# Kernel tuning notes

Measured on AMD Instinct MI355X. Metric: run time of the kernel, lower is better.

Reference implementation:

```python
import jax, jax.numpy as jnp
import numpy as np

def setup_inputs() -> dict:
    key = jax.random.key(0)
    k1, k2, k3 = jax.random.split(key, 3)
    B, L, H, E = 2, 2048, 16, 64
    queries = jax.random.normal(k1, (B, L, H, E), dtype=jnp.float32)
    keys = jax.random.normal(k2, (B, L, H, E), dtype=jnp.float32)
    values = jax.random.normal(k3, (B, L, H, E), dtype=jnp.float32)
    return {"queries": queries, "keys": keys, "values": values}

def reference(queries, keys, values):
    B, L, H, E = queries.shape
    S = keys.shape[1]
    scale = 1.0 / jnp.sqrt(jnp.asarray(E, dtype=queries.dtype))
    # scores: [B, H, L, S]
    scores = jnp.einsum('blhe,bshe->bhls', queries, keys)
    # causal mask: position l attends to s <= l (TriangularCausalMask triu diag=1 is masked)
    causal = jnp.tril(jnp.ones((L, S), dtype=bool))  # True = keep
    scores = jnp.where(causal[None, None, :, :], scores, -jnp.inf)
    A = jax.nn.softmax(scale * scores, axis=-1)
    # dropout is identity in eval / p=0
    V = jnp.einsum('bhls,bshd->blhd', A, values)
    return V
```

## Files before the change

kernel.cpp:

```cpp
#include <hip/hip_runtime.h>
#include <hip/hip_bf16.h>

typedef __attribute__((ext_vector_type(8))) short short8;
typedef __attribute__((ext_vector_type(4))) float f32x4;
typedef __attribute__((ext_vector_type(2))) unsigned uint2v;

#define MFMA16(a, b, c) __builtin_amdgcn_mfma_f32_16x16x32_bf16((a), (b), (c), 0, 0, 0)

constexpr int Bc = 2, Lc = 2048, Hc = 16, Ec = 64;
constexpr float LOG2E = 1.4426950408889634f;
constexpr float SCALE2 = 0.125f * LOG2E;
constexpr float NEGBIG = -3.0e38f;

union SW { short8 s8; unsigned u[4]; float4 f4; };

__device__ __forceinline__ unsigned cvtpk(float lo, float hi) {
  unsigned r;
  asm("v_cvt_pk_bf16_f32 %0, %1, %2" : "=v"(r) : "v"(lo), "v"(hi));
  return r;
}
__device__ __forceinline__ float exp2v(float x) {
  float r;
  asm("v_exp_f32 %0, %1" : "=v"(r) : "v"(x));
  return r;
}
__device__ __forceinline__ void plswap32(unsigned& a, unsigned& b) {
  uint2v r = __builtin_amdgcn_permlane32_swap(a, b, false, false);
  a = r[0]; b = r[1];
}
__device__ __forceinline__ void plswap16(unsigned& a, unsigned& b) {
  uint2v r = __builtin_amdgcn_permlane16_swap(a, b, false, false);
  a = r[0]; b = r[1];
}
__device__ __forceinline__ float bflymax(float x) {
  unsigned a = __builtin_bit_cast(unsigned, x), b = a;
  plswap16(a, b);
  float y = fmaxf(__builtin_bit_cast(float, a), __builtin_bit_cast(float, b));
  a = __builtin_bit_cast(unsigned, y); b = a;
  plswap32(a, b);
  return fmaxf(__builtin_bit_cast(float, a), __builtin_bit_cast(float, b));
}

__global__ __launch_bounds__(256)
void prep(const float* __restrict__ K, const float* __restrict__ V,
          uint4* __restrict__ Kb, unsigned short* __restrict__ Vt) {
  const int bid = blockIdx.x;
  const int t = threadIdx.x;
  if (bid < 2048) {
    const int i = bid * 256 + t;
    const float4* s = reinterpret_cast<const float4*>(K) + (size_t)i * 2;
    float4 a = s[0], b = s[1];
    uint4 o;
    o.x = cvtpk(a.x, a.y); o.y = cvtpk(a.z, a.w);
    o.z = cvtpk(b.x, b.y); o.w = cvtpk(b.z, b.w);
    Kb[i] = o;
  } else {
    const int vw = (bid - 2048) * 4 + (t >> 6);
    const int l = t & 63;
    const int bh = vw >> 7;
    const int s0 = (vw & 127) * 16;
    const float* vp = V + ((size_t)(bh >> 4) * Lc + s0) * (Hc * Ec) +
                      (bh & 15) * Ec + l;
    float va[16];
    #pragma unroll
    for (int j = 0; j < 16; ++j) va[j] = vp[j * (Hc * Ec)];
    uint4 o0, o1;
    o0.x = cvtpk(va[0], va[1]);   o0.y = cvtpk(va[2], va[3]);
    o0.z = cvtpk(va[4], va[5]);   o0.w = cvtpk(va[6], va[7]);
    o1.x = cvtpk(va[8], va[9]);   o1.y = cvtpk(va[10], va[11]);
    o1.z = cvtpk(va[12], va[13]); o1.w = cvtpk(va[14], va[15]);
    uint4* dst = reinterpret_cast<uint4*>(Vt + ((size_t)vw * 64 + l) * 16);
    dst[0] = o0;
    dst[1] = o1;
  }
}

__global__ __launch_bounds__(512, 2)
void attn_fwd(const float* __restrict__ Qg, const unsigned short* __restrict__ Kb,
              const unsigned short* __restrict__ Vt, float* __restrict__ Og) {
  __shared__ __align__(16) short kt2[2][8192];
  __shared__ __align__(16) float mscr[64 * 68 + 128];

  const int bid = blockIdx.x;
  const int pair = bid >> 5;
  const int bh = bid & 31;
  const int h = bh & (Hc - 1);
  const int b = bh >> 4;
  const int iLo = pair;
  const int QbL = iLo * 64;
  const int QbH = (31 - pair) * 64;
  const int RL = (iLo + 2) >> 1;

  const int t = threadIdx.x;
  const int w = t >> 6;
  const int qsub = w & 3;
  const int par = w >> 2;
  const int l = t & 63;
  const int n = l & 15;
  const int g = l >> 4;
  const int sp4 = ((g & 1) << 3) | ((g >> 1) << 2);

  const f32x4 zero4 = {0.f, 0.f, 0.f, 0.f};
  short8 onesv;
  #pragma unroll
  for (int j = 0; j < 8; ++j) onesv[j] = (short)0x3F80;

  short8 qf[2];
  auto loadq = [&](int Qb) {
    const int q = Qb + qsub * 16 + n;
    const float* qp = Qg + ((size_t)(b * Lc + q) * Hc + h) * Ec + g * 8;
    SW a0, a1, b0, b1, r0, r1;
    a0.f4 = reinterpret_cast<const float4*>(qp)[0];
    a1.f4 = reinterpret_cast<const float4*>(qp)[1];
    b0.f4 = reinterpret_cast<const float4*>(qp + 32)[0];
    b1.f4 = reinterpret_cast<const float4*>(qp + 32)[1];
    r0.u[0] = cvtpk(a0.f4.x * SCALE2, a0.f4.y * SCALE2);
    r0.u[1] = cvtpk(a0.f4.z * SCALE2, a0.f4.w * SCALE2);
    r0.u[2] = cvtpk(a1.f4.x * SCALE2, a1.f4.y * SCALE2);
    r0.u[3] = cvtpk(a1.f4.z * SCALE2, a1.f4.w * SCALE2);
    r1.u[0] = cvtpk(b0.f4.x * SCALE2, b0.f4.y * SCALE2);
    r1.u[1] = cvtpk(b0.f4.z * SCALE2, b0.f4.w * SCALE2);
    r1.u[2] = cvtpk(b1.f4.x * SCALE2, b1.f4.y * SCALE2);
    r1.u[3] = cvtpk(b1.f4.z * SCALE2, b1.f4.w * SCALE2);
    qf[0] = r0.s8;
    qf[1] = r1.s8;
  };

  f32x4 acc[4] = {zero4, zero4, zero4, zero4};
  float mrun = NEGBIG, lrun = 0.f;

  const int srow = t >> 2;
  const int prow = (srow & ~12) | ((srow & 4) << 1) | ((srow & 8) >> 1);
  const int kc0 = (t & 3) * 16;

  float4 kA, kB;

  auto issueK = [&](int r0) {
    unsigned koff = (unsigned)((((b * Lc + r0 + srow) * Hc + h) * Ec + kc0) * 2);
    asm volatile(
      "global_load_dwordx4 %[k0], %[ko], %[kb]\n\t"
      "global_load_dwordx4 %[k1], %[ko], %[kb] offset:16"
      : [k0]"=v"(kA), [k1]"=v"(kB)
      : [ko]"v"(koff), [kb]"s"(Kb)
      : "memory");
  };
  auto commit = [&](int buf) {
    asm volatile("s_waitcnt vmcnt(0)" ::: "memory");
    __builtin_amdgcn_sched_barrier(0);
    short* kt = kt2[buf];
    *reinterpret_cast<short8*>(&kt[(prow * 64 + kc0) ^ ((prow & 7) << 3)]) =
        *reinterpret_cast<short8*>(&kA);
    *reinterpret_cast<short8*>(&kt[(prow * 64 + kc0 + 8) ^ ((prow & 7) << 3)]) =
        *reinterpret_cast<short8*>(&kB);
  };

  auto round = [&](int Qb, int str, int curb, bool pre, int nstrK) {
    const int sb = str * 128 + par * 64;
    const int qtop = Qb + qsub * 16;
    if (sb > qtop + 15) {
      if (pre) issueK(nstrK * 128);
      return;
    }
    const short* ktb = kt2[curb];

    f32x4 sc[4] = {zero4, zero4, zero4, zero4};
    __builtin_amdgcn_s_setprio(1);
    #pragma unroll
    for (int kc = 0; kc < 2; ++kc) {
      #pragma unroll
      for (int cb = 0; cb < 4; ++cb) {
        const int row = par * 64 + cb * 16 + n;
        const int idx = (row * 64 + kc * 32 + g * 8) ^ ((n & 7) << 3);
        short8 kf = *reinterpret_cast<const short8*>(&ktb[idx]);
        sc[cb] = MFMA16(kf, qf[kc], sc[cb]);
      }
    }
    __builtin_amdgcn_s_setprio(0);

    SW vr0[4], vr1[4];
    {
      unsigned a0 = (unsigned)((((bh * 128 + str * 8 + par * 4 + (g >> 1)) * 64 + n) * 32)
                               + ((g & 1) * 16));
      unsigned a1 = a0 + 4096;
      asm volatile(
        "global_load_dwordx4 %[f0], %[a0], %[vb]\n\t"
        "global_load_dwordx4 %[f1], %[a0], %[vb] offset:512\n\t"
        "global_load_dwordx4 %[f2], %[a0], %[vb] offset:1024\n\t"
        "global_load_dwordx4 %[f3], %[a0], %[vb] offset:1536\n\t"
        "global_load_dwordx4 %[f4], %[a1], %[vb]\n\t"
        "global_load_dwordx4 %[f5], %[a1], %[vb] offset:512\n\t"
        "global_load_dwordx4 %[f6], %[a1], %[vb] offset:1024\n\t"
        "global_load_dwordx4 %[f7], %[a1], %[vb] offset:1536"
        : [f0]"=v"(vr0[0].f4), [f1]"=v"(vr0[1].f4), [f2]"=v"(vr0[2].f4), [f3]"=v"(vr0[3].f4),
          [f4]"=v"(vr1[0].f4), [f5]"=v"(vr1[1].f4), [f6]"=v"(vr1[2].f4), [f7]"=v"(vr1[3].f4)
        : [a0]"v"(a0), [a1]"v"(a1), [vb]"s"(Vt)
        : "memory");
    }
    if (pre) issueK(nstrK * 128);

    const int qg = qtop + n;
    if (sb + 63 > qtop) {
      #pragma unroll
      for (int cb = 0; cb < 4; ++cb)
        #pragma unroll
        for (int r = 0; r < 4; ++r)
          if (sb + cb * 16 + sp4 + r > qg) sc[cb][r] = NEGBIG;
    }

    float m8 = fmaxf(fmaxf(fmaxf(sc[0][0], sc[0][1]), fmaxf(sc[0][2], sc[0][3])),
                     fmaxf(fmaxf(sc[1][0], sc[1][1]), fmaxf(sc[1][2], sc[1][3])));
    m8 = fmaxf(m8, fmaxf(fmaxf(fmaxf(sc[2][0], sc[2][1]), fmaxf(sc[2][2], sc[2][3])),
                         fmaxf(fmaxf(sc[3][0], sc[3][1]), fmaxf(sc[3][2], sc[3][3]))));
    m8 = bflymax(m8);

    const bool resc = !__all(m8 <= mrun);
    if (resc) {
      const float mn = fmaxf(mrun, m8);
      const float afac = exp2v(mrun - mn);
      mrun = mn;
      lrun *= afac;
      #pragma unroll
      for (int e4 = 0; e4 < 4; ++e4)
        #pragma unroll
        for (int r = 0; r < 4; ++r) acc[e4][r] *= afac;
    }

    unsigned ua[4], ub[4];
    #pragma unroll
    for (int cb = 0; cb < 4; ++cb) {
      ua[cb] = cvtpk(exp2v(sc[cb][0] - mrun), exp2v(sc[cb][1] - mrun));
      ub[cb] = cvtpk(exp2v(sc[cb][2] - mrun), exp2v(sc[cb][3] - mrun));
    }
    plswap32(ua[0], ua[1]);
    plswap32(ub[0], ub[1]);
    plswap32(ua[2], ua[3]);
    plswap32(ub[2], ub[3]);
    SW pw0, pw1;
    pw0.u[0] = ua[0]; pw0.u[1] = ub[0]; pw0.u[2] = ua[1]; pw0.u[3] = ub[1];
    pw1.u[0] = ua[2]; pw1.u[1] = ub[2]; pw1.u[2] = ua[3]; pw1.u[3] = ub[3];

    if (pre) asm volatile("s_waitcnt vmcnt(2)" ::: "memory");
    else     asm volatile("s_waitcnt vmcnt(0)" ::: "memory");
    __builtin_amdgcn_sched_barrier(0);

    __builtin_amdgcn_s_setprio(1);
    #pragma unroll
    for (int e4 = 0; e4 < 4; ++e4) {
      acc[e4] = MFMA16(vr0[e4].s8, pw0.s8, acc[e4]);
      acc[e4] = MFMA16(vr1[e4].s8, pw1.s8, acc[e4]);
    }
    f32x4 rs = MFMA16(onesv, pw0.s8, zero4);
    rs = MFMA16(onesv, pw1.s8, rs);
    __builtin_amdgcn_s_setprio(0);
    lrun += rs[0];
  };

  auto merge_store = [&](int Qb) {
    __syncthreads();
    const int row = qsub * 16 + n;
    if (par == 1) {
      float* base = mscr + row * 68;
      #pragma unroll
      for (int e4 = 0; e4 < 4; ++e4)
        #pragma unroll
        for (int r = 0; r < 4; ++r) base[e4 * 16 + g * 4 + r] = acc[e4][r];
      if (g == 0) {
        mscr[64 * 68 + row] = mrun;
        mscr[64 * 68 + 64 + row] = lrun;
      }
    }
    __syncthreads();
    if (par == 0) {
      const float* base = mscr + row * 68;
      const float m1 = mscr[64 * 68 + row];
      const float l1 = mscr[64 * 68 + 64 + row];
      const float mm = fmaxf(mrun, m1);
      const float a0 = exp2v(mrun - mm);
      const float a1 = exp2v(m1 - mm);
      const float inv = 1.0f / (lrun * a0 + l1 * a1);
      const int q = Qb + row;
      float* op = Og + ((size_t)(b * Lc + q) * Hc + h) * Ec;
      #pragma unroll
      for (int e4 = 0; e4 < 4; ++e4) {
        float4 v;
        v.x = (acc[e4][0] * a0 + base[e4 * 16 + g * 4 + 0] * a1) * inv;
        v.y = (acc[e4][1] * a0 + base[e4 * 16 + g * 4 + 1] * a1) * inv;
        v.z = (acc[e4][2] * a0 + base[e4 * 16 + g * 4 + 2] * a1) * inv;
        v.w = (acc[e4][3] * a0 + base[e4 * 16 + g * 4 + 3] * a1) * inv;
        *reinterpret_cast<float4*>(op + e4 * 16 + g * 4) = v;
      }
    }
  };

  constexpr int NRO = 17;
  loadq(QbL);
  issueK(0);
  commit(0);
  __syncthreads();

  int cur = 0;
  for (int rd = 0; rd < NRO; ++rd) {
    const bool pre = (rd + 1 < NRO);
    const int nrd = rd + 1;
    const int nstr = (nrd < RL) ? nrd : nrd - RL;
    const bool lo = (rd < RL);
    round(lo ? QbL : QbH, lo ? rd : rd - RL, cur, pre, nstr);
    if (rd == RL - 1) {
      merge_store(QbL);
      #pragma unroll
      for (int e4 = 0; e4 < 4; ++e4) acc[e4] = zero4;
      mrun = NEGBIG;
      lrun = 0.f;
      loadq(QbH);
    }
    if (pre) commit(cur ^ 1);
    __syncthreads();
    cur ^= 1;
  }

  merge_store(QbH);
}

extern "C" void kernel_launch(void* const* d_in, const int* in_sizes, int n_in,
                              void* d_out, int out_size, void* d_ws, size_t ws_size,
                              hipStream_t stream) {
  const float* Q = (const float*)d_in[0];
  const float* K = (const float*)d_in[1];
  const float* V = (const float*)d_in[2];
  float* O = (float*)d_out;
  unsigned short* Kb = (unsigned short*)d_ws;
  unsigned short* Vt = (unsigned short*)((char*)d_ws + (size_t)Bc * Lc * Hc * Ec * 2);
  prep<<<dim3(3072), dim3(256), 0, stream>>>(K, V, (uint4*)Kb, Vt);
  dim3 grid(Bc * Hc * 16);
  attn_fwd<<<grid, dim3(512), 0, stream>>>(Q, Kb, Vt, O);
}
```

Measured before the change: 50.38 us.

## Load K fragments directly from pre-swizzled global layout, drop LDS staging

The prep kernel now writes K in a fragment-ready bf16 layout so each wave loads its MFMA operands straight into registers, removing the shared-memory double buffer and the per-round block barriers. K and V loads are software-pipelined one round ahead with vmcnt waits, and the skipped-tile path still issues prefetches. This trades LDS traffic and syncthreads for more VGPRs held in flight and more redundant global/L2 reads of K across the waves sharing a block.

```diff
diff --git a/kernel.cpp b/kernel.cpp
--- a/kernel.cpp
+++ b/kernel.cpp
@@ -43,20 +43,31 @@
 
 __global__ __launch_bounds__(256)
 void prep(const float* __restrict__ K, const float* __restrict__ V,
-          uint4* __restrict__ Kb, unsigned short* __restrict__ Vt) {
+          uint4* __restrict__ Kc, unsigned short* __restrict__ Vt) {
   const int bid = blockIdx.x;
   const int t = threadIdx.x;
-  if (bid < 2048) {
-    const int i = bid * 256 + t;
-    const float4* s = reinterpret_cast<const float4*>(K) + (size_t)i * 2;
-    float4 a = s[0], b = s[1];
-    uint4 o;
-    o.x = cvtpk(a.x, a.y); o.y = cvtpk(a.z, a.w);
-    o.z = cvtpk(b.x, b.y); o.w = cvtpk(b.z, b.w);
-    Kb[i] = o;
+  const int l = t & 63;
+  if (bid < 1024) {
+    const int vw = bid * 4 + (t >> 6);
+    const int bh = vw >> 7;
+    const int c = vw & 127;
+    const int j = l >> 4, nn = l & 15;
+    const int pnn = (nn & 3) | ((nn & 4) << 1) | ((nn & 8) >> 1);
+    const float* kp = K + ((size_t)((bh >> 4) * Lc + c * 16 + pnn) * Hc +
+                           (bh & 15)) * Ec + j * 8;
+    float4 x0 = reinterpret_cast<const float4*>(kp)[0];
+    float4 x1 = reinterpret_cast<const float4*>(kp)[1];
+    float4 y0 = reinterpret_cast<const float4*>(kp + 32)[0];
+    float4 y1 = reinterpret_cast<const float4*>(kp + 32)[1];
+    uint4 ox, oy;
+    ox.x = cvtpk(x0.x, x0.y); ox.y = cvtpk(x0.z, x0.w);
+    ox.z = cvtpk(x1.x, x1.y); ox.w = cvtpk(x1.z, x1.w);
+    oy.x = cvtpk(y0.x, y0.y); oy.y = cvtpk(y0.z, y0.w);
+    oy.z = cvtpk(y1.x, y1.y); oy.w = cvtpk(y1.z, y1.w);
+    Kc[(size_t)vw * 128 + l] = ox;
+    Kc[(size_t)vw * 128 + l + 64] = oy;
   } else {
-    const int vw = (bid - 2048) * 4 + (t >> 6);
-    const int l = t & 63;
+    const int vw = (bid - 1024) * 4 + (t >> 6);
     const int bh = vw >> 7;
     const int s0 = (vw & 127) * 16;
     const float* vp = V + ((size_t)(bh >> 4) * Lc + s0) * (Hc * Ec) +
@@ -76,9 +87,8 @@
 }
 
 __global__ __launch_bounds__(512, 2)
-void attn_fwd(const float* __restrict__ Qg, const unsigned short* __restrict__ Kb,
+void attn_fwd(const float* __restrict__ Qg, const unsigned short* __restrict__ Kc,
               const unsigned short* __restrict__ Vt, float* __restrict__ Og) {
-  __shared__ __align__(16) short kt2[2][8192];
   __shared__ __align__(16) float mscr[64 * 68 + 128];
 
   const int bid = blockIdx.x;
@@ -129,130 +139,130 @@
   f32x4 acc[4] = {zero4, zero4, zero4, zero4};
   float mrun = NEGBIG, lrun = 0.f;
 
-  const int srow = t >> 2;
-  const int prow = (srow & ~12) | ((srow & 4) << 1) | ((srow & 8) >> 1);
-  const int kc0 = (t & 3) * 16;
-
-  float4 kA, kB;
-
-  auto issueK = [&](int r0) {
-    unsigned koff = (unsigned)((((b * Lc + r0 + srow) * Hc + h) * Ec + kc0) * 2);
+  SW kr[4][2];
+  SW vr0[4], vr1[4];
+
+  auto issueK = [&](int str) {
+    unsigned a0 = (unsigned)((((bh * 128 + str * 8 + par * 4) * 128) + (g * 16 + n)) * 16);
+    unsigned a1 = a0 + 4096;
     asm volatile(
-      "global_load_dwordx4 %[k0], %[ko], %[kb]\n\t"
-      "global_load_dwordx4 %[k1], %[ko], %[kb] offset:16"
-      : [k0]"=v"(kA), [k1]"=v"(kB)
-      : [ko]"v"(koff), [kb]"s"(Kb)
+      "global_load_dwordx4 %[r0], %[a0], %[kb]\n\t"
+      "global_load_dwordx4 %[r1], %[a0], %[kb] offset:1024\n\t"
+      "global_load_dwordx4 %[r2], %[a0], %[kb] offset:2048\n\t"
+      "global_load_dwordx4 %[r3], %[a0], %[kb] offset:3072\n\t"
+      "global_load_dwordx4 %[r4], %[a1], %[kb]\n\t"
+      "global_load_dwordx4 %[r5], %[a1], %[kb] offset:1024\n\t"
+      "global_load_dwordx4 %[r6], %[a1], %[kb] offset:2048\n\t"
+      "global_load_dwordx4 %[r7], %[a1], %[kb] offset:3072"
+      : [r0]"=&v"(kr[0][0].f4), [r1]"=&v"(kr[0][1].f4),
+        [r2]"=&v"(kr[1][0].f4), [r3]"=&v"(kr[1][1].f4),
+        [r4]"=&v"(kr[2][0].f4), [r5]"=&v"(kr[2][1].f4),
+        [r6]"=&v"(kr[3][0].f4), [r7]"=&v"(kr[3][1].f4)
+      : [a0]"v"(a0), [a1]"v"(a1), [kb]"s"(Kc)
       : "memory");
   };
-  auto commit = [&](int buf) {
-    asm volatile("s_waitcnt vmcnt(0)" ::: "memory");
-    __builtin_amdgcn_sched_barrier(0);
-    short* kt = kt2[buf];
-    *reinterpret_cast<short8*>(&kt[(prow * 64 + kc0) ^ ((prow & 7) << 3)]) =
-        *reinterpret_cast<short8*>(&kA);
-    *reinterpret_cast<short8*>(&kt[(prow * 64 + kc0 + 8) ^ ((prow & 7) << 3)]) =
-        *reinterpret_cast<short8*>(&kB);
-  };
-
-  auto round = [&](int Qb, int str, int curb, bool pre, int nstrK) {
+  auto issueV = [&](int str) {
+    unsigned a0 = (unsigned)((((bh * 128 + str * 8 + par * 4 + (g >> 1)) * 64 + n) * 32)
+                             + ((g & 1) * 16));
+    unsigned a1 = a0 + 4096;
+    asm volatile(
+      "global_load_dwordx4 %[f0], %[a0], %[vb]\n\t"
+      "global_load_dwordx4 %[f1], %[a0], %[vb] offset:512\n\t"
+      "global_load_dwordx4 %[f2], %[a0], %[vb] offset:1024\n\t"
+      "global_load_dwordx4 %[f3], %[a0], %[vb] offset:1536\n\t"
+      "global_load_dwordx4 %[f4], %[a1], %[vb]\n\t"
+      "global_load_dwordx4 %[f5], %[a1], %[vb] offset:512\n\t"
+      "global_load_dwordx4 %[f6], %[a1], %[vb] offset:1024\n\t"
+      "global_load_dwordx4 %[f7], %[a1], %[vb] offset:1536"
+      : [f0]"=&v"(vr0[0].f4), [f1]"=&v"(vr0[1].f4),
+        [f2]"=&v"(vr0[2].f4), [f3]"=&v"(vr0[3].f4),
+        [f4]"=&v"(vr1[0].f4), [f5]"=&v"(vr1[1].f4),
+        [f6]"=&v"(vr1[2].f4), [f7]"=&v"(vr1[3].f4)
+      : [a0]"v"(a0), [a1]"v"(a1), [vb]"s"(Vt)
+      : "memory");
+  };
+
+  auto round = [&](int Qb, int str, bool pre, int nstrN) {
     const int sb = str * 128 + par * 64;
     const int qtop = Qb + qsub * 16;
-    if (sb > qtop + 15) {
-      if (pre) issueK(nstrK * 128);
-      return;
-    }
-    const short* ktb = kt2[curb];
+    const bool active = (sb <= qtop + 15);
+
+    asm volatile("s_waitcnt vmcnt(8)" ::: "memory");
+    __builtin_amdgcn_sched_barrier(0);
 
     f32x4 sc[4] = {zero4, zero4, zero4, zero4};
-    __builtin_amdgcn_s_setprio(1);
-    #pragma unroll
-    for (int kc = 0; kc < 2; ++kc) {
+    if (active) {
+      __builtin_amdgcn_s_setprio(1);
+      #pragma unroll
+      for (int kc = 0; kc < 2; ++kc)
+        #pragma unroll
+        for (int cb = 0; cb < 4; ++cb)
+          sc[cb] = MFMA16(kr[cb][kc].s8, qf[kc], sc[cb]);
+      __builtin_amdgcn_s_setprio(0);
+    }
+    if (pre) issueK(nstrN);
+
+    SW pw0, pw1;
+    pw0.f4 = float4{0, 0, 0, 0};
+    pw1.f4 = float4{0, 0, 0, 0};
+    if (active) {
+      const int qg = qtop + n;
+      if (sb + 63 > qtop) {
+        #pragma unroll
+        for (int cb = 0; cb < 4; ++cb)
+          #pragma unroll
+          for (int r = 0; r < 4; ++r)
+            if (sb + cb * 16 + sp4 + r > qg) sc[cb][r] = NEGBIG;
+      }
+      float m8 = fmaxf(fmaxf(fmaxf(sc[0][0], sc[0][1]), fmaxf(sc[0][2], sc[0][3])),
+                       fmaxf(fmaxf(sc[1][0], sc[1][1]), fmaxf(sc[1][2], sc[1][3])));
+      m8 = fmaxf(m8, fmaxf(fmaxf(fmaxf(sc[2][0], sc[2][1]), fmaxf(sc[2][2], sc[2][3])),
+                           fmaxf(fmaxf(sc[3][0], sc[3][1]), fmaxf(sc[3][2], sc[3][3]))));
+      m8 = bflymax(m8);
+
+      const bool resc = !__all(m8 <= mrun);
+      if (resc) {
+        const float mn = fmaxf(mrun, m8);
+        const float afac = exp2v(mrun - mn);
+        mrun = mn;
+        lrun *= afac;
+        #pragma unroll
+        for (int e4 = 0; e4 < 4; ++e4)
+          #pragma unroll
+          for (int r = 0; r < 4; ++r) acc[e4][r] *= afac;
+      }
+
+      unsigned ua[4], ub[4];
       #pragma unroll
       for (int cb = 0; cb < 4; ++cb) {
-        const int row = par * 64 + cb * 16 + n;
-        const int idx = (row * 64 + kc * 32 + g * 8) ^ ((n & 7) << 3);
-        short8 kf = *reinterpret_cast<const short8*>(&ktb[idx]);
-        sc[cb] = MFMA16(kf, qf[kc], sc[cb]);
-      }
-    }
-    __builtin_amdgcn_s_setprio(0);
-
-    SW vr0[4], vr1[4];
-    {
-      unsigned a0 = (unsigned)((((bh * 128 + str * 8 + par * 4 + (g >> 1)) * 64 + n) * 32)
-                               + ((g & 1) * 16));
-      unsigned a1 = a0 + 4096;
-      asm volatile(
-        "global_load_dwordx4 %[f0], %[a0], %[vb]\n\t"
-        "global_load_dwordx4 %[f1], %[a0], %[vb] offset:512\n\t"
-        "global_load_dwordx4 %[f2], %[a0], %[vb] offset:1024\n\t"
-        "global_load_dwordx4 %[f3], %[a0], %[vb] offset:1536\n\t"
-        "global_load_dwordx4 %[f4], %[a1], %[vb]\n\t"
-        "global_load_dwordx4 %[f5], %[a1], %[vb] offset:512\n\t"
-        "global_load_dwordx4 %[f6], %[a1], %[vb] offset:1024\n\t"
-        "global_load_dwordx4 %[f7], %[a1], %[vb] offset:1536"
-        : [f0]"=v"(vr0[0].f4), [f1]"=v"(vr0[1].f4), [f2]"=v"(vr0[2].f4), [f3]"=v"(vr0[3].f4),
-          [f4]"=v"(vr1[0].f4), [f5]"=v"(vr1[1].f4), [f6]"=v"(vr1[2].f4), [f7]"=v"(vr1[3].f4)
-        : [a0]"v"(a0), [a1]"v"(a1), [vb]"s"(Vt)
-        : "memory");
-    }
-    if (pre) issueK(nstrK * 128);
-
-    const int qg = qtop + n;
-    if (sb + 63 > qtop) {
-      #pragma unroll
-      for (int cb = 0; cb < 4; ++cb)
-        #pragma unroll
-        for (int r = 0; r < 4; ++r)
-          if (sb + cb * 16 + sp4 + r > qg) sc[cb][r] = NEGBIG;
-    }
-
-    float m8 = fmaxf(fmaxf(fmaxf(sc[0][0], sc[0][1]), fmaxf(sc[0][2], sc[0][3])),
-                     fmaxf(fmaxf(sc[1][0], sc[1][1]), fmaxf(sc[1][2], sc[1][3])));
-    m8 = fmaxf(m8, fmaxf(fmaxf(fmaxf(sc[2][0], sc[2][1]), fmaxf(sc[2][2], sc[2][3])),
-                         fmaxf(fmaxf(sc[3][0], sc[3][1]), fmaxf(sc[3][2], sc[3][3]))));
-    m8 = bflymax(m8);
-
-    const bool resc = !__all(m8 <= mrun);
-    if (resc) {
-      const float mn = fmaxf(mrun, m8);
-      const float afac = exp2v(mrun - mn);
-      mrun = mn;
-      lrun *= afac;
-      #pragma unroll
-      for (int e4 = 0; e4 < 4; ++e4)
-        #pragma unroll
-        for (int r = 0; r < 4; ++r) acc[e4][r] *= afac;
-    }
-
-    unsigned ua[4], ub[4];
-    #pragma unroll
-    for (int cb = 0; cb < 4; ++cb) {
-      ua[cb] = cvtpk(exp2v(sc[cb][0] - mrun), exp2v(sc[cb][1] - mrun));
-      ub[cb] = cvtpk(exp2v(sc[cb][2] - mrun), exp2v(sc[cb][3] - mrun));
-    }
-    plswap32(ua[0], ua[1]);
-    plswap32(ub[0], ub[1]);
-    plswap32(ua[2], ua[3]);
-    plswap32(ub[2], ub[3]);
-    SW pw0, pw1;
-    pw0.u[0] = ua[0]; pw0.u[1] = ub[0]; pw0.u[2] = ua[1]; pw0.u[3] = ub[1];
-    pw1.u[0] = ua[2]; pw1.u[1] = ub[2]; pw1.u[2] = ua[3]; pw1.u[3] = ub[3];
-
-    if (pre) asm volatile("s_waitcnt vmcnt(2)" ::: "memory");
-    else     asm volatile("s_waitcnt vmcnt(0)" ::: "memory");
+        ua[cb] = cvtpk(exp2v(sc[cb][0] - mrun), exp2v(sc[cb][1] - mrun));
+        ub[cb] = cvtpk(exp2v(sc[cb][2] - mrun), exp2v(sc[cb][3] - mrun));
+      }
+      plswap32(ua[0], ua[1]);
+      plswap32(ub[0], ub[1]);
+      plswap32(ua[2], ua[3]);
+      plswap32(ub[2], ub[3]);
+      pw0.u[0] = ua[0]; pw0.u[1] = ub[0]; pw0.u[2] = ua[1]; pw0.u[3] = ub[1];
+      pw1.u[0] = ua[2]; pw1.u[1] = ub[2]; pw1.u[2] = ua[3]; pw1.u[3] = ub[3];
+    }
+
+    if (pre) { asm volatile("s_waitcnt vmcnt(8)" ::: "memory"); }
+    else     { asm volatile("s_waitcnt vmcnt(0)" ::: "memory"); }
     __builtin_amdgcn_sched_barrier(0);
 
-    __builtin_amdgcn_s_setprio(1);
-    #pragma unroll
-    for (int e4 = 0; e4 < 4; ++e4) {
-      acc[e4] = MFMA16(vr0[e4].s8, pw0.s8, acc[e4]);
-      acc[e4] = MFMA16(vr1[e4].s8, pw1.s8, acc[e4]);
-    }
-    f32x4 rs = MFMA16(onesv, pw0.s8, zero4);
-    rs = MFMA16(onesv, pw1.s8, rs);
-    __builtin_amdgcn_s_setprio(0);
-    lrun += rs[0];
+    if (active) {
+      __builtin_amdgcn_s_setprio(1);
+      #pragma unroll
+      for (int e4 = 0; e4 < 4; ++e4) {
+        acc[e4] = MFMA16(vr0[e4].s8, pw0.s8, acc[e4]);
+        acc[e4] = MFMA16(vr1[e4].s8, pw1.s8, acc[e4]);
+      }
+      f32x4 rs = MFMA16(onesv, pw0.s8, zero4);
+      rs = MFMA16(onesv, pw1.s8, rs);
+      __builtin_amdgcn_s_setprio(0);
+      lrun += rs[0];
+    }
+    if (pre) issueV(nstrN);
   };
 
   auto merge_store = [&](int Qb) {
@@ -295,27 +305,24 @@
   constexpr int NRO = 17;
   loadq(QbL);
   issueK(0);
-  commit(0);
-  __syncthreads();
-
-  int cur = 0;
+  issueV(0);
+
   for (int rd = 0; rd < NRO; ++rd) {
     const bool pre = (rd + 1 < NRO);
     const int nrd = rd + 1;
     const int nstr = (nrd < RL) ? nrd : nrd - RL;
     const bool lo = (rd < RL);
-    round(lo ? QbL : QbH, lo ? rd : rd - RL, cur, pre, nstr);
+    round(lo ? QbL : QbH, lo ? rd : rd - RL, pre, nstr);
     if (rd == RL - 1) {
       merge_store(QbL);
       #pragma unroll
       for (int e4 = 0; e4 < 4; ++e4) acc[e4] = zero4;
       mrun = NEGBIG;
       lrun = 0.f;
+      asm volatile("s_waitcnt vmcnt(0)" ::: "memory");
+      __builtin_amdgcn_sched_barrier(0);
       loadq(QbH);
     }
-    if (pre) commit(cur ^ 1);
-    __syncthreads();
-    cur ^= 1;
   }
 
   merge_store(QbH);
@@ -328,9 +335,9 @@
   const float* K = (const float*)d_in[1];
   const float* V = (const float*)d_in[2];
   float* O = (float*)d_out;
-  unsigned short* Kb = (unsigned short*)d_ws;
+  unsigned short* Kc = (unsigned short*)d_ws;
   unsigned short* Vt = (unsigned short*)((char*)d_ws + (size_t)Bc * Lc * Hc * Ec * 2);
-  prep<<<dim3(3072), dim3(256), 0, stream>>>(K, V, (uint4*)Kb, Vt);
+  prep<<<dim3(2048), dim3(256), 0, stream>>>(K, V, (uint4*)Kc, Vt);
   dim3 grid(Bc * Hc * 16);
-  attn_fwd<<<grid, dim3(512), 0, stream>>>(Q, Kb, Vt, O);
-}
+  attn_fwd<<<grid, dim3(512), 0, stream>>>(Q, Kc, Vt, O);
+}
```

Result: slower. 56.01 us (+11.2%).
